# Optimization experiments

Hardware: AMD Instinct MI355X
Metric: run time of the kernel (lower is better)

Reference implementation:

```python
import jax, jax.numpy as jnp
import numpy as np

B, S, Q, D = 8, 2048, 2048, 1024  # additive path requires S == Q


def setup_inputs() -> dict:
    key = jax.random.key(0)
    ks = jax.random.split(key, 5)
    def glorot(k, shape):
        fan_in, fan_out = shape[0], shape[1]
        limit = np.sqrt(6.0 / (fan_in + fan_out)).astype(np.float32)
        return jax.random.uniform(k, shape, jnp.float32, -limit, limit)
    return {
        "source": jax.random.normal(ks[0], (B, S, D), jnp.float32),
        "query": jax.random.normal(ks[1], (B, Q, D), jnp.float32),
        "kernel": glorot(ks[2], (S, Q)),
        "wk_kernel": glorot(ks[3], (D, Q)),
        "wq_kernel": glorot(ks[4], (S, D)),
    }


def reference(source, query, kernel, wk_kernel, wq_kernel):
    # query permuted to (B, D, Q) as in call()
    q_t = jnp.transpose(query, (0, 2, 1))
    # additive similarity: tanh(Wk . Source + Wq . Query) . kernel
    f_att = (jnp.einsum("bsd,dq->bsq", source, wk_kernel)
             + jnp.einsum("sd,bdq->bsq", wq_kernel, q_t))  # (B, S, Q)
    sim = jnp.einsum("bsq,qt->bst", jnp.tanh(f_att), kernel)  # (B, S, Q)
    sm = jax.nn.softmax(sim, axis=-1)  # softmax over last axis (Keras default)
    # sm_t = permute(sm, (0,2,1)); result = batch_dot(sm_t, Source)
    return jnp.einsum("bsq,bsd->bqd", sm, source)  # (B, Q, D)
```

## Files before the change

kernel.cpp:

```cpp
#include <hip/hip_runtime.h>
#include <hip/hip_bf16.h>
#include <stdint.h>

typedef unsigned short u16;

#define B_ 8
#define S_ 2048
#define Q_ 2048
#define D_ 1024
#define T_ 2048

typedef __attribute__((ext_vector_type(8))) short short8;
typedef __attribute__((ext_vector_type(4))) float f32x4;

__device__ __forceinline__ u16 f2b(float f) {
  union { float f; uint32_t u; } x; x.f = f;
  uint32_t r = x.u + 0x7fffu + ((x.u >> 16) & 1u);
  return (u16)(r >> 16);
}
__device__ __forceinline__ float b2f(u16 h) {
  union { uint32_t u; float f; } x; x.u = ((uint32_t)h) << 16;
  return x.f;
}
__device__ __forceinline__ float tanh_fast(float x) {
  return 1.0f - 2.0f / (__expf(2.0f * x) + 1.0f);
}
__device__ __forceinline__ void async16(const void* g, void* l) {
  __builtin_amdgcn_global_load_lds(
      (const __attribute__((address_space(1))) void*)g,
      (__attribute__((address_space(3))) void*)l, 16, 0, 0);
}

__global__ void cast_f32_bf16_k(const float* __restrict__ in, u16* __restrict__ out, int n4) {
  int i = blockIdx.x * 256 + threadIdx.x;
  if (i >= n4) return;
  float4 v = ((const float4*)in)[i];
  uint32_t lo = (uint32_t)f2b(v.x) | ((uint32_t)f2b(v.y) << 16);
  uint32_t hi = (uint32_t)f2b(v.z) | ((uint32_t)f2b(v.w) << 16);
  ((uint2*)out)[i] = make_uint2(lo, hi);
}

__global__ void transpose_f32_bf16_v(const float* __restrict__ in, u16* __restrict__ out,
                                     int R, int C) {
  __shared__ u16 t[64 * 72];
  int z = blockIdx.z;
  const float* pin = in + (size_t)z * R * C;
  u16* pout = out + (size_t)z * R * C;
  int c0 = blockIdx.x * 64, r0 = blockIdx.y * 64;
  int tid = threadIdx.x;
  int rr = tid >> 4, c4 = (tid & 15) * 4;
#pragma unroll
  for (int p = 0; p < 4; ++p) {
    int r = p * 16 + rr;
    float4 v = *(const float4*)&pin[(size_t)(r0 + r) * C + c0 + c4];
    t[(c4 + 0) * 72 + r] = f2b(v.x);
    t[(c4 + 1) * 72 + r] = f2b(v.y);
    t[(c4 + 2) * 72 + r] = f2b(v.z);
    t[(c4 + 3) * 72 + r] = f2b(v.w);
  }
  __syncthreads();
  int ct = tid >> 3, r8 = (tid & 7) * 8;
#pragma unroll
  for (int p = 0; p < 2; ++p) {
    int c = p * 32 + ct;
    uint2 lo = *(const uint2*)&t[c * 72 + r8];
    uint2 hi = *(const uint2*)&t[c * 72 + r8 + 4];
    *(uint4*)&pout[(size_t)(c0 + c) * R + r0 + r8] = make_uint4(lo.x, lo.y, hi.x, hi.y);
  }
}

__global__ void src_prep_v(const float* __restrict__ in, u16* __restrict__ outc,
                           u16* __restrict__ outT) {
  __shared__ u16 t[64 * 72];
  int z = blockIdx.z;
  const float* pin = in + (size_t)z * S_ * D_;
  u16* pc = outc + (size_t)z * S_ * D_;
  u16* pt = outT + (size_t)z * S_ * D_;
  int c0 = blockIdx.x * 64, r0 = blockIdx.y * 64;
  int tid = threadIdx.x;
  int rr = tid >> 4, c4 = (tid & 15) * 4;
#pragma unroll
  for (int p = 0; p < 4; ++p) {
    int r = p * 16 + rr;
    float4 v = *(const float4*)&pin[(size_t)(r0 + r) * D_ + c0 + c4];
    u16 b0 = f2b(v.x), b1 = f2b(v.y), b2 = f2b(v.z), b3 = f2b(v.w);
    uint2 pk;
    pk.x = (uint32_t)b0 | ((uint32_t)b1 << 16);
    pk.y = (uint32_t)b2 | ((uint32_t)b3 << 16);
    *(uint2*)&pc[(size_t)(r0 + r) * D_ + c0 + c4] = pk;
    t[(c4 + 0) * 72 + r] = b0;
    t[(c4 + 1) * 72 + r] = b1;
    t[(c4 + 2) * 72 + r] = b2;
    t[(c4 + 3) * 72 + r] = b3;
  }
  __syncthreads();
  int ct = tid >> 3, r8 = (tid & 7) * 8;
#pragma unroll
  for (int p = 0; p < 2; ++p) {
    int c = p * 32 + ct;
    uint2 lo = *(const uint2*)&t[c * 72 + r8];
    uint2 hi = *(const uint2*)&t[c * 72 + r8 + 4];
    *(uint4*)&pt[(size_t)(c0 + c) * S_ + r0 + r8] = make_uint4(lo.x, lo.y, hi.x, hi.y);
  }
}

__global__ void scale_srcT_k(u16* __restrict__ srcT, const float* __restrict__ l) {
  size_t i = (size_t)blockIdx.x * 256 + threadIdx.x;
  size_t e0 = i * 8;
  int s8 = (int)(e0 & (S_ - 1));
  int bb = (int)(e0 / ((size_t)D_ * S_));
  const float* lp = l + (size_t)bb * S_ + s8;
  float4 l0 = *(const float4*)lp;
  float4 l1 = *(const float4*)(lp + 4);
  uint4 raw = *(uint4*)&srcT[e0];
  uint32_t w[4] = {raw.x, raw.y, raw.z, raw.w};
  float li[8] = {l0.x, l0.y, l0.z, l0.w, l1.x, l1.y, l1.z, l1.w};
  uint32_t o[4];
#pragma unroll
  for (int k = 0; k < 4; ++k) {
    float a = b2f((u16)(w[k] & 0xffffu)) / li[2 * k];
    float b = b2f((u16)(w[k] >> 16)) / li[2 * k + 1];
    o[k] = (uint32_t)f2b(a) | ((uint32_t)f2b(b) << 16);
  }
  *(uint4*)&srcT[e0] = make_uint4(o[0], o[1], o[2], o[3]);
}

__global__ __launch_bounds__(512, 2) void gemm256_k(
    const u16* __restrict__ A1, long lda1, long bsA1,
    const u16* __restrict__ B1, long ldb1, long bsB1,
    const u16* __restrict__ A2, long lda2, long bsA2,
    const u16* __restrict__ B2, long ldb2, long bsB2,
    void* __restrict__ Cv, long ldc, long bsC,
    int K, int Srows, int nTerms, int mode, float* __restrict__ lsum) {
  __shared__ __align__(16) u16 lds[65536];

  const int tid = threadIdx.x;
  const int w = tid >> 6, lane = tid & 63;
  const int wr = w >> 2, wc = w & 3;
  const int l15 = lane & 15, lhi4 = lane >> 4;

  const int gx = gridDim.x;
  const int nwg = gx * (int)gridDim.y;
  int lid = blockIdx.y * gx + blockIdx.x;
  if ((nwg & 7) == 0) lid = (lid & 7) * (nwg >> 3) + (lid >> 3);
  const int bn = lid % gx, bm = lid / gx;
  const int n0 = bn * 256, m0 = bm * 256;
  const int b = m0 / Srows;
  const int s0 = m0 - b * Srows;

  const int ktiles = K >> 6;
  const int ktlog = __ffs(ktiles) - 1;
  const int ktmask = ktiles - 1;
  const int NT = nTerms * ktiles;

  const u16* gA1 = A1 + (size_t)bsA1 * b + (size_t)s0 * lda1;
  const u16* gB1 = B1 + (size_t)bsB1 * b + (size_t)n0 * ldb1;
  const u16* gA2 = (nTerms > 1) ? (A2 + (size_t)bsA2 * b + (size_t)s0 * lda2) : gA1;
  const u16* gB2 = (nTerms > 1) ? (B2 + (size_t)bsB2 * b + (size_t)n0 * ldb2) : gB1;

  auto STG = [&](int tile, int isB, int half) {
    if (tile >= NT) return;
    const int term = tile >> ktlog;
    const int kt = (tile & ktmask) << 6;
    const u16* g = isB ? (term ? gB2 : gB1) : (term ? gA2 : gA1);
    const long ld = isB ? (term ? ldb2 : ldb1) : (term ? lda2 : lda1);
    u16* lb = lds + (tile & 1) * 32768 + isB * 16384;
#pragma unroll
    for (int is = 0; is < 2; ++is) {
      const int bi = is * 8 + w;
      int s, kk;
      if (isB) { s = (bi >> 2) * 4 + half * 2 + (bi & 1); kk = (bi >> 1) & 1; }
      else     { s = half * 4 + (bi & 3) + (bi >> 3) * 8; kk = (bi >> 2) & 1; }
      async16(g + (size_t)(s * 16 + l15) * ld + kt + kk * 32 + lhi4 * 8,
              lb + s * 1024 + kk * 512);
    }
  };

  f32x4 acc[8][4];
#pragma unroll
  for (int x = 0; x < 8; ++x)
#pragma unroll
    for (int y = 0; y < 4; ++y)
#pragma unroll
      for (int r = 0; r < 4; ++r) acc[x][y][r] = 0.0f;

  u16* bufXA = lds;
  u16* bufXB = lds + 16384;
  u16* bufYA = lds + 32768;
  u16* bufYB = lds + 49152;

  const int lof = lane * 8;

  short8 av[4][2], bv[2][2][2];

#define RD_A(bufA, mh)                                                         \
  _Pragma("unroll") for (int kk = 0; kk < 2; ++kk)                             \
  _Pragma("unroll") for (int fr = 0; fr < 4; ++fr)                             \
      av[fr][kk] =                                                             \
          *(const short8*)&(bufA)[(wr * 8 + (mh)*4 + fr) * 1024 + kk * 512 + lof];
#define RD_B_ALL(bufB)                                                         \
  _Pragma("unroll") for (int bp = 0; bp < 2; ++bp)                             \
  _Pragma("unroll") for (int fc = 0; fc < 2; ++fc)                             \
  _Pragma("unroll") for (int kk = 0; kk < 2; ++kk)                             \
      bv[bp][fc][kk] =                                                         \
          *(const short8*)&(bufB)[(wc * 4 + bp * 2 + fc) * 1024 + kk * 512 + lof];
#define BAR __builtin_amdgcn_s_barrier()
#define SB0 __builtin_amdgcn_sched_barrier(0)
#define LGKM0 asm volatile("s_waitcnt lgkmcnt(0)")
#define VMC4 asm volatile("s_waitcnt vmcnt(4)" ::: "memory")
#define VMC0 asm volatile("s_waitcnt vmcnt(0)" ::: "memory")
#define MFMA16(mh, bp)                                                         \
  __builtin_amdgcn_s_setprio(1);                                               \
  _Pragma("unroll") for (int kk = 0; kk < 2; ++kk)                             \
  _Pragma("unroll") for (int fr = 0; fr < 4; ++fr)                             \
  _Pragma("unroll") for (int fc = 0; fc < 2; ++fc)                             \
      acc[(mh)*4 + fr][(bp)*2 + fc] = __builtin_amdgcn_mfma_f32_16x16x32_bf16( \
          av[fr][kk], bv[bp][fc][kk], acc[(mh)*4 + fr][(bp)*2 + fc], 0, 0, 0); \
  __builtin_amdgcn_s_setprio(0)

  STG(0, 0, 0); STG(0, 1, 1); STG(0, 0, 1); STG(0, 1, 0);
  STG(1, 0, 0); STG(1, 1, 1);
  VMC4;
  BAR; SB0;

  const int niter = NT >> 1;
  for (int i = 0; i + 1 < niter; ++i) {
    const int u = 2 * i;
    RD_A(bufXA, 0); RD_B_ALL(bufXB);
    STG(u + 1, 0, 1);
    BAR; LGKM0; SB0;
    MFMA16(0, 0);
    BAR;

    STG(u + 1, 1, 0);
    BAR; LGKM0; SB0;
    MFMA16(0, 1);
    BAR;

    RD_A(bufXA, 1);
    STG(u + 2, 0, 0);
    BAR; LGKM0; SB0;
    MFMA16(1, 1);
    BAR;

    STG(u + 2, 1, 1);
    BAR; LGKM0; SB0;
    MFMA16(1, 0);
    VMC4;
    BAR; SB0;

    RD_A(bufYA, 0); RD_B_ALL(bufYB);
    STG(u + 2, 0, 1);
    BAR; LGKM0; SB0;
    MFMA16(0, 0);
    BAR;

    STG(u + 2, 1, 0);
    BAR; LGKM0; SB0;
    MFMA16(0, 1);
    BAR;

    RD_A(bufYA, 1);
    STG(u + 3, 0, 0);
    BAR; LGKM0; SB0;
    MFMA16(1, 1);
    BAR;

    STG(u + 3, 1, 1);
    BAR; LGKM0; SB0;
    MFMA16(1, 0);
    VMC4;
    BAR; SB0;
  }

  {
    RD_A(bufXA, 0); RD_B_ALL(bufXB);
    STG(NT - 1, 0, 1);
    BAR; LGKM0; SB0;
    MFMA16(0, 0);
    BAR;

    STG(NT - 1, 1, 0);
    BAR; LGKM0; SB0;
    MFMA16(0, 1);
    BAR;

    RD_A(bufXA, 1);
    BAR; LGKM0; SB0;
    MFMA16(1, 1);
    BAR;

    BAR; LGKM0; SB0;
    MFMA16(1, 0);
    VMC0;
    BAR; SB0;

    RD_A(bufYA, 0); RD_B_ALL(bufYB);
    BAR; LGKM0; SB0;
    MFMA16(0, 0);
    BAR;

    BAR; LGKM0; SB0;
    MFMA16(0, 1);
    BAR;

    RD_A(bufYA, 1);
    BAR; LGKM0; SB0;
    MFMA16(1, 1);
    BAR;

    BAR; LGKM0; SB0;
    MFMA16(1, 0);
  }

  if (mode == 3) {
#pragma unroll
    for (int fr = 0; fr < 8; ++fr)
#pragma unroll
      for (int fc = 0; fc < 4; ++fc)
#pragma unroll
        for (int r = 0; r < 4; ++r) acc[fr][fc][r] = __expf(acc[fr][fc][r]);
    float* lrowp = lsum + (size_t)b * Srows + s0;
#pragma unroll
    for (int fr = 0; fr < 8; ++fr)
#pragma unroll
      for (int r = 0; r < 4; ++r) {
        float pv = acc[fr][0][r] + acc[fr][1][r] + acc[fr][2][r] + acc[fr][3][r];
        pv += __shfl_xor(pv, 1);
        pv += __shfl_xor(pv, 2);
        pv += __shfl_xor(pv, 4);
        pv += __shfl_xor(pv, 8);
        if (l15 == 0) {
          const int row = wr * 128 + fr * 16 + lhi4 * 4 + r;
          atomicAdd(&lrowp[row], pv);
        }
      }
    u16* gP = (u16*)Cv + (size_t)bsC * b + (size_t)n0 * ldc + s0;
    __syncthreads();
#pragma unroll
    for (int p = 0; p < 2; ++p) {
      if ((wc >> 1) == p) {
#pragma unroll
        for (int fr = 0; fr < 8; ++fr)
#pragma unroll
          for (int fc = 0; fc < 4; ++fc) {
            const int tc = (wc & 1) * 64 + fc * 16 + l15;
            const int sl = wr * 128 + fr * 16 + lhi4 * 4;
            u16 p0 = f2b(acc[fr][fc][0]);
            u16 p1 = f2b(acc[fr][fc][1]);
            u16 p2 = f2b(acc[fr][fc][2]);
            u16 p3 = f2b(acc[fr][fc][3]);
            uint2 pk;
            pk.x = (uint32_t)p0 | ((uint32_t)p1 << 16);
            pk.y = (uint32_t)p2 | ((uint32_t)p3 << 16);
            *(uint2*)&lds[tc * 268 + sl] = pk;
          }
      }
      __syncthreads();
#pragma unroll
      for (int j = 0; j < 8; ++j) {
        const int idx = j * 512 + tid;
        const int tt = idx >> 5, s8 = (idx & 31) * 8;
        uint2 lo = *(const uint2*)&lds[tt * 268 + s8];
        uint2 h2 = *(const uint2*)&lds[tt * 268 + s8 + 4];
        *(uint4*)&gP[(size_t)(p * 128 + tt) * ldc + s8] =
            make_uint4(lo.x, lo.y, h2.x, h2.y);
      }
      __syncthreads();
    }
    return;
  }

  const size_t cb = (size_t)bsC * b + (size_t)s0 * ldc + n0;
  if (mode == 2) {
    float* C = (float*)Cv + cb;
#pragma unroll
    for (int fr = 0; fr < 8; ++fr)
#pragma unroll
      for (int fc = 0; fc < 4; ++fc) {
        const int col = wc * 64 + fc * 16 + l15;
#pragma unroll
        for (int r = 0; r < 4; ++r) {
          const int row = wr * 128 + fr * 16 + lhi4 * 4 + r;
          C[(size_t)row * ldc + col] = acc[fr][fc][r];
        }
      }
  } else {
    u16* C = (u16*)Cv + cb;
#pragma unroll
    for (int fr = 0; fr < 8; ++fr)
#pragma unroll
      for (int fc = 0; fc < 4; ++fc) {
        const int col = wc * 64 + fc * 16 + l15;
#pragma unroll
        for (int r = 0; r < 4; ++r) {
          const int row = wr * 128 + fr * 16 + lhi4 * 4 + r;
          float v = acc[fr][fc][r];
          if (mode == 0) v = tanh_fast(v);
          C[(size_t)row * ldc + col] = f2b(v);
        }
      }
  }
}

#undef RD_A
#undef RD_B_ALL
#undef BAR
#undef SB0
#undef LGKM0
#undef VMC4
#undef VMC0
#undef MFMA16

extern "C" void kernel_launch(void* const* d_in, const int* in_sizes, int n_in,
                              void* d_out, int out_size, void* d_ws, size_t ws_size,
                              hipStream_t stream) {
  const float* src = (const float*)d_in[0];
  const float* qry = (const float*)d_in[1];
  const float* ker = (const float*)d_in[2];
  const float* wk  = (const float*)d_in[3];
  const float* wq  = (const float*)d_in[4];
  float* out = (float*)d_out;
  u16* ws = (u16*)d_ws;

  u16* srcb  = ws;
  u16* qryb  = srcb  + (size_t)B_ * S_ * D_;
  u16* wqb   = qryb  + (size_t)B_ * Q_ * D_;
  u16* wkT   = wqb   + (size_t)S_ * D_;
  u16* kerT  = wkT   + (size_t)D_ * Q_;
  u16* srcT  = kerT  + (size_t)Q_ * T_;
  u16* tanhT = srcT  + (size_t)B_ * D_ * S_;
  u16* PT    = tanhT + (size_t)B_ * S_ * Q_;
  float* l   = (float*)(PT + (size_t)B_ * T_ * S_);

  dim3 tb(256);

  cast_f32_bf16_k<<<(B_ * Q_ * D_) / 1024, 256, 0, stream>>>(qry, qryb, (B_ * Q_ * D_) / 4);
  cast_f32_bf16_k<<<(S_ * D_) / 1024, 256, 0, stream>>>(wq, wqb, (S_ * D_) / 4);
  transpose_f32_bf16_v<<<dim3(Q_ / 64, D_ / 64, 1), tb, 0, stream>>>(wk, wkT, D_, Q_);
  transpose_f32_bf16_v<<<dim3(T_ / 64, Q_ / 64, 1), tb, 0, stream>>>(ker, kerT, Q_, T_);
  src_prep_v<<<dim3(D_ / 64, S_ / 64, B_), tb, 0, stream>>>(src, srcb, srcT);
  hipMemsetAsync(l, 0, (size_t)B_ * S_ * sizeof(float), stream);

  gemm256_k<<<dim3(Q_ / 256, (B_ * S_) / 256), 512, 0, stream>>>(
      srcb, D_, (long)S_ * D_,
      wkT, D_, 0,
      wqb, D_, 0,
      qryb, D_, (long)Q_ * D_,
      tanhT, Q_, (long)S_ * Q_,
      D_, S_, 2, 0, nullptr);

  gemm256_k<<<dim3(T_ / 256, (B_ * S_) / 256), 512, 0, stream>>>(
      tanhT, Q_, (long)S_ * Q_,
      kerT, Q_, 0,
      nullptr, 0, 0, nullptr, 0, 0,
      PT, S_, (long)T_ * S_,
      Q_, S_, 1, 3, l);

  scale_srcT_k<<<(B_ * D_ * S_) / (256 * 8), 256, 0, stream>>>(srcT, l);

  gemm256_k<<<dim3(D_ / 256, (B_ * T_) / 256), 512, 0, stream>>>(
      PT, S_, (long)T_ * S_,
      srcT, S_, (long)D_ * S_,
      nullptr, 0, 0, nullptr, 0, 0,
      out, D_, (long)T_ * D_,
      S_, T_, 1, 2, nullptr);
}
```

Before: 585.6 us.

## Reorder GEMM stage loads and deepen prefetch, drop sched barriers and redundant waits

Reorders the global-to-LDS staging of the GEMM half-tiles so one more stage is issued before the first barrier. The vmcnt wait is relaxed from 4 to 6 outstanding loads. All sched_barrier fences are removed, and the LDS-count waits before MFMA blocks that do not follow fresh LDS reads are dropped. The aim is more overlap between memory loads and MFMA, and more freedom for the compiler scheduler. The cost is a higher risk of LDS buffer hazards or worse instruction interleaving.

New measurement: 584.2 us. About the same (-0.2%).

```diff
diff --git a/kernel.cpp b/kernel.cpp
--- a/kernel.cpp
+++ b/kernel.cpp
@@ -205,9 +205,8 @@
       bv[bp][fc][kk] =                                                         \
           *(const short8*)&(bufB)[(wc * 4 + bp * 2 + fc) * 1024 + kk * 512 + lof];
 #define BAR __builtin_amdgcn_s_barrier()
-#define SB0 __builtin_amdgcn_sched_barrier(0)
 #define LGKM0 asm volatile("s_waitcnt lgkmcnt(0)")
-#define VMC4 asm volatile("s_waitcnt vmcnt(4)" ::: "memory")
+#define VMC6 asm volatile("s_waitcnt vmcnt(6)" ::: "memory")
 #define VMC0 asm volatile("s_waitcnt vmcnt(0)" ::: "memory")
 #define MFMA16(mh, bp)                                                         \
   __builtin_amdgcn_s_setprio(1);                                               \
@@ -218,98 +217,83 @@
           av[fr][kk], bv[bp][fc][kk], acc[(mh)*4 + fr][(bp)*2 + fc], 0, 0, 0); \
   __builtin_amdgcn_s_setprio(0)
 
-  STG(0, 0, 0); STG(0, 1, 1); STG(0, 0, 1); STG(0, 1, 0);
-  STG(1, 0, 0); STG(1, 1, 1);
-  VMC4;
-  BAR; SB0;
+  STG(0, 0, 0); STG(0, 1, 0); STG(0, 0, 1); STG(0, 1, 1);
+  STG(1, 0, 0); STG(1, 1, 1); STG(1, 0, 1);
+  VMC6;
+  BAR;
 
   const int niter = NT >> 1;
   for (int i = 0; i + 1 < niter; ++i) {
     const int u = 2 * i;
     RD_A(bufXA, 0); RD_B_ALL(bufXB);
-    STG(u + 1, 0, 1);
-    BAR; LGKM0; SB0;
+    STG(u + 1, 1, 0);
+    BAR; LGKM0;
     MFMA16(0, 0);
     BAR;
-
-    STG(u + 1, 1, 0);
-    BAR; LGKM0; SB0;
+    STG(u + 2, 0, 0);
+    BAR;
     MFMA16(0, 1);
     BAR;
-
     RD_A(bufXA, 1);
-    STG(u + 2, 0, 0);
-    BAR; LGKM0; SB0;
+    STG(u + 2, 1, 1);
+    BAR; LGKM0;
     MFMA16(1, 1);
     BAR;
-
-    STG(u + 2, 1, 1);
-    BAR; LGKM0; SB0;
+    STG(u + 2, 0, 1);
+    BAR;
     MFMA16(1, 0);
-    VMC4;
-    BAR; SB0;
-
+    VMC6;
+    BAR;
     RD_A(bufYA, 0); RD_B_ALL(bufYB);
-    STG(u + 2, 0, 1);
-    BAR; LGKM0; SB0;
+    STG(u + 2, 1, 0);
+    BAR; LGKM0;
     MFMA16(0, 0);
     BAR;
-
-    STG(u + 2, 1, 0);
-    BAR; LGKM0; SB0;
+    STG(u + 3, 0, 0);
+    BAR;
     MFMA16(0, 1);
     BAR;
-
     RD_A(bufYA, 1);
-    STG(u + 3, 0, 0);
-    BAR; LGKM0; SB0;
+    STG(u + 3, 1, 1);
+    BAR; LGKM0;
     MFMA16(1, 1);
     BAR;
-
-    STG(u + 3, 1, 1);
-    BAR; LGKM0; SB0;
+    STG(u + 3, 0, 1);
+    BAR;
     MFMA16(1, 0);
-    VMC4;
-    BAR; SB0;
+    VMC6;
+    BAR;
   }
 
   {
     RD_A(bufXA, 0); RD_B_ALL(bufXB);
-    STG(NT - 1, 0, 1);
-    BAR; LGKM0; SB0;
+    STG(NT - 1, 1, 0);
+    BAR; LGKM0;
     MFMA16(0, 0);
     BAR;
-
-    STG(NT - 1, 1, 0);
-    BAR; LGKM0; SB0;
+    BAR;
     MFMA16(0, 1);
     BAR;
-
     RD_A(bufXA, 1);
-    BAR; LGKM0; SB0;
+    BAR; LGKM0;
     MFMA16(1, 1);
     BAR;
-
-    BAR; LGKM0; SB0;
+    BAR;
     MFMA16(1, 0);
     VMC0;
-    BAR; SB0;
-
+    BAR;
     RD_A(bufYA, 0); RD_B_ALL(bufYB);
-    BAR; LGKM0; SB0;
+    BAR; LGKM0;
     MFMA16(0, 0);
     BAR;
-
-    BAR; LGKM0; SB0;
+    BAR;
     MFMA16(0, 1);
     BAR;
-
     RD_A(bufYA, 1);
-    BAR; LGKM0; SB0;
+    BAR; LGKM0;
     MFMA16(1, 1);
     BAR;
-
-    BAR; LGKM0; SB0;
+    BAR;
     MFMA16(1, 0);
   }
 
@@ -406,9 +390,8 @@
 #undef RD_A
 #undef RD_B_ALL
 #undef BAR
-#undef SB0
 #undef LGKM0
-#undef VMC4
+#undef VMC6
 #undef VMC0
 #undef MFMA16
 
```
